# Performance work log

Measured on AMD Instinct MI355X. Metric: run time of the kernel, lower is better.

The kernel has to match this reference:

```python
import jax, jax.numpy as jnp
import numpy as np

RADIUS = 3
T_STEPS = 2
NEG = -9.0e8
B, L, DEG = 256, 64, 6
FEAT, BOND, FP, OUT = 39, 10, 256, 1


def _leaky(x):
    return jax.nn.leaky_relu(x, 0.01)


def _gru(x, h, wih, whh, bih, bhh):
    # PyTorch GRUCell: gates ordered (r, z, n)
    gi = x @ wih.T + bih
    gh = h @ whh.T + bhh
    ir, iz, inn = jnp.split(gi, 3, axis=-1)
    hr, hz, hn = jnp.split(gh, 3, axis=-1)
    r = jax.nn.sigmoid(ir + hr)
    z = jax.nn.sigmoid(iz + hz)
    n = jnp.tanh(inn + r * hn)
    return (1.0 - z) * n + z * h


def _forward(atom_list, bond_list, atom_mask,
             atom_fc_w, atom_fc_b, neighbor_fc_w, neighbor_fc_b,
             align_w, align_b, attend_w, attend_b,
             gru_wih, gru_whh, gru_bih, gru_bhh,
             mol_align_w, mol_align_b, mol_attend_w, mol_attend_b,
             mol_gru_wih, mol_gru_whh, mol_gru_bih, mol_gru_bhh,
             out_w, out_b,
             atom_degree_list, bond_degree_list):
    b, l, _ = atom_list.shape
    mask = atom_mask[..., None]                                   # [B,L,1]
    atom_feature = _leaky(atom_list @ atom_fc_w.T + atom_fc_b)    # [B,L,FP]

    # per-molecule neighbor gather (padding index = L-1)
    bidx = jnp.arange(b)[:, None, None]
    atom_nb = atom_list[bidx, atom_degree_list]                    # [B,L,deg,FEAT]
    bond_nb = bond_list[bidx, bond_degree_list]                    # [B,L,deg,BOND]
    neighbor_feature = _leaky(
        jnp.concatenate([atom_nb, bond_nb], axis=-1) @ neighbor_fc_w.T + neighbor_fc_b
    )                                                              # [B,L,deg,FP]

    attend_mask = (atom_degree_list != l - 1).astype(atom_feature.dtype)[..., None]
    softmax_mask = jnp.where(atom_degree_list == l - 1, NEG, 0.0).astype(atom_feature.dtype)[..., None]

    for d in range(RADIUS):
        af_exp = jnp.broadcast_to(atom_feature[:, :, None, :], neighbor_feature.shape)
        feature_align = jnp.concatenate([af_exp, neighbor_feature], axis=-1)  # [B,L,deg,2FP]
        align_score = _leaky(feature_align @ align_w[d].T + align_b[d]) + softmax_mask
        attention_weight = jax.nn.softmax(align_score, axis=-2) * attend_mask
        attended = neighbor_feature @ attend_w[d].T + attend_b[d]
        context = jax.nn.elu(jnp.sum(attention_weight * attended, axis=-2))   # [B,L,FP]
        atom_feature = _gru(context.reshape(b * l, -1), atom_feature.reshape(b * l, -1),
                            gru_wih[d], gru_whh[d], gru_bih[d], gru_bhh[d]).reshape(b, l, -1)
        # faithful to original: self-feature broadcast across neighbor dim
        neighbor_feature = jnp.broadcast_to(jax.nn.relu(atom_feature)[:, :, None, :],
                                            neighbor_feature.shape)

    mol_feature = jnp.sum(jax.nn.relu(atom_feature) * mask, axis=-2)          # [B,FP]
    mol_softmax_mask = jnp.where(atom_mask == 0, NEG, 0.0).astype(atom_feature.dtype)[..., None]

    for _ in range(T_STEPS):
        m_exp = jnp.broadcast_to(mol_feature[:, None, :], atom_feature.shape)
        mol_align = jnp.concatenate([m_exp, atom_feature], axis=-1)           # [B,L,2FP]
        mol_score = _leaky(mol_align @ mol_align_w.T + mol_align_b) + mol_softmax_mask
        mol_w = jax.nn.softmax(mol_score, axis=-2) * mask
        attended = atom_feature @ mol_attend_w.T + mol_attend_b
        mol_context = jax.nn.elu(jnp.sum(mol_w * attended, axis=-2))
        mol_feature = _gru(mol_context, mol_feature,
                           mol_gru_wih, mol_gru_whh, mol_gru_bih, mol_gru_bhh)

    mol_prediction = mol_feature @ out_w.T + out_b
    return atom_feature, mol_prediction


def setup_inputs() -> dict:
    key = jax.random.key(0)
    ks = jax.random.split(key, 20)
    s = 0.05
    return {
        "atom_list": jax.random.normal(ks[0], (B, L, FEAT), jnp.float32),
        "bond_list": jax.random.normal(ks[1], (B, L, BOND), jnp.float32),
        "atom_degree_list": jax.random.randint(ks[2], (B, L, DEG), 0, L),
        "bond_degree_list": jax.random.randint(ks[3], (B, L, DEG), 0, L),
        "atom_mask": jnp.ones((B, L), jnp.float32),
        "atom_fc_w": jax.random.normal(ks[4], (FP, FEAT)) * s,
        "atom_fc_b": jnp.zeros((FP,)),
        "neighbor_fc_w": jax.random.normal(ks[5], (FP, FEAT + BOND)) * s,
        "neighbor_fc_b": jnp.zeros((FP,)),
        "align_w": jax.random.normal(ks[6], (RADIUS, 1, 2 * FP)) * s,
        "align_b": jnp.zeros((RADIUS, 1)),
        "attend_w": jax.random.normal(ks[7], (RADIUS, FP, FP)) * s,
        "attend_b": jnp.zeros((RADIUS, FP)),
        "gru_wih": jax.random.normal(ks[8], (RADIUS, 3 * FP, FP)) * s,
        "gru_whh": jax.random.normal(ks[9], (RADIUS, 3 * FP, FP)) * s,
        "gru_bih": jnp.zeros((RADIUS, 3 * FP)),
        "gru_bhh": jnp.zeros((RADIUS, 3 * FP)),
        "mol_align_w": jax.random.normal(ks[10], (1, 2 * FP)) * s,
        "mol_align_b": jnp.zeros((1,)),
        "mol_attend_w": jax.random.normal(ks[11], (FP, FP)) * s,
        "mol_attend_b": jnp.zeros((FP,)),
        "mol_gru_wih": jax.random.normal(ks[12], (3 * FP, FP)) * s,
        "mol_gru_whh": jax.random.normal(ks[13], (3 * FP, FP)) * s,
        "mol_gru_bih": jnp.zeros((3 * FP,)),
        "mol_gru_bhh": jnp.zeros((3 * FP,)),
        "out_w": jax.random.normal(ks[14], (OUT, FP)) * s,
        "out_b": jnp.zeros((OUT,)),
    }


def reference(atom_list, bond_list, atom_degree_list, bond_degree_list, atom_mask,
              atom_fc_w, atom_fc_b, neighbor_fc_w, neighbor_fc_b,
              align_w, align_b, attend_w, attend_b,
              gru_wih, gru_whh, gru_bih, gru_bhh,
              mol_align_w, mol_align_b, mol_attend_w, mol_attend_b,
              mol_gru_wih, mol_gru_whh, mol_gru_bih, mol_gru_bhh,
              out_w, out_b):
    return _forward(atom_list, bond_list, atom_mask,
                    atom_fc_w, atom_fc_b, neighbor_fc_w, neighbor_fc_b,
                    align_w, align_b, attend_w, attend_b,
                    gru_wih, gru_whh, gru_bih, gru_bhh,
                    mol_align_w, mol_align_b, mol_attend_w, mol_attend_b,
                    mol_gru_wih, mol_gru_whh, mol_gru_bih, mol_gru_bhh,
                    out_w, out_b,
                    atom_degree_list, bond_degree_list)
```

## Files before the change

kernel.cpp:

```cpp
#include <hip/hip_runtime.h>
#include <hip/hip_bf16.h>

#define NB 256
#define NL 64
#define DEG 6
#define FEAT 39
#define BOND 10
#define FP 256
#define NEGV (-9.0e8f)

using s16x8 = __attribute__((ext_vector_type(8))) short;
using f32x4 = __attribute__((ext_vector_type(4))) float;

__device__ __forceinline__ unsigned short f2bf(float f){
  unsigned u = __float_as_uint(f);
  u += 0x7fffu + ((u >> 16) & 1u);
  return (unsigned short)(u >> 16);
}
__device__ __forceinline__ float lo16(unsigned u){ return __uint_as_float(u << 16); }
__device__ __forceinline__ float hi16(unsigned u){ return __uint_as_float(u & 0xffff0000u); }

__device__ __forceinline__ float block_sum256(float v, float* scr){
  #pragma unroll
  for(int o=32;o>0;o>>=1) v += __shfl_down(v, o, 64);
  __syncthreads();
  if((threadIdx.x & 63) == 0) scr[threadIdx.x >> 6] = v;
  __syncthreads();
  return scr[0] + scr[1] + scr[2] + scr[3];
}
__device__ __forceinline__ float wave_allsum(float v){
  #pragma unroll
  for(int o=1;o<64;o<<=1) v += __shfl_xor(v, o, 64);
  return v;
}

#define MCVT_N0 65536
#define MCVT_N1 196608
#define MCVT_N2 196608
#define MCVT_TOT (MCVT_N0+MCVT_N1+MCVT_N2)
#define CTXPK_N (3*8*8192)
#define GPK_N   (3*2*8*24576)
#define HALF_U16 24576

__global__ void k_cvt_mol(const float* __restrict__ a0, const float* __restrict__ a1,
                          const float* __restrict__ a2, unsigned short* __restrict__ dst){
  int i = blockIdx.x*256 + threadIdx.x;
  if(i >= MCVT_TOT) return;
  int off = i; const float* src;
  if(off < MCVT_N0) src = a0;
  else { off -= MCVT_N0;
    if(off < MCVT_N1) src = a1;
    else { off -= MCVT_N1; src = a2; } }
  dst[i] = f2bf(src[off]);
}

__global__ void k_pack(const float* __restrict__ attend_w, const float* __restrict__ gru_wih,
                       const float* __restrict__ gru_whh,
                       unsigned short* __restrict__ ctx_pk, unsigned short* __restrict__ gates_pk){
  int i = blockIdx.x*256 + threadIdx.x;
  if(i < CTXPK_N){
    int d = i >> 16;
    int rem = i & 65535;
    int kk = rem >> 13;
    int r2 = rem & 8191;
    int g = r2 >> 9;
    int l = (r2 >> 3) & 63;
    int q = r2 & 7;
    int row = g*16 + (l & 15);
    int k = kk*32 + (l >> 4)*8 + q;
    ctx_pk[i] = f2bf(attend_w[((size_t)d*256 + row)*256 + k]);
  } else {
    int j = i - CTXPK_N;
    if(j >= GPK_N) return;
    int d = j / 393216;
    int rem = j - d*393216;
    int nc = rem / 196608; rem -= nc*196608;
    int kk = rem / 24576;  rem -= kk*24576;
    int f = rem >> 9;
    int l = (rem >> 3) & 63;
    int q = rem & 7;
    int s = f >> 3, g = f & 7;
    int row = nc*128 + g*16 + (l & 15);
    int k = kk*32 + (l >> 4)*8 + q;
    float v = (s < 3) ? gru_wih[(((size_t)d*3 + s)*256 + row)*256 + k]
                      : gru_whh[(((size_t)d*3 + (s-3))*256 + row)*256 + k];
    gates_pk[j] = f2bf(v);
  }
}

__global__ void k_tr(const float* __restrict__ aw, const float* __restrict__ nw,
                     float* __restrict__ afcT, unsigned short* __restrict__ nfcT){
  int i = blockIdx.x*256 + threadIdx.x;
  if(i < 40*256){
    int k = i >> 8, r = i & 255;
    afcT[i] = (k < FEAT) ? aw[r*FEAT + k] : 0.f;
  } else {
    int j = i - 40*256;
    int k = j >> 8, r = j & 255;
    nfcT[j] = (k < FEAT+BOND) ? f2bf(nw[r*(FEAT+BOND) + k]) : (unsigned short)0;
  }
}

__global__ __launch_bounds__(256) void k_atom4(const float* __restrict__ atom,
    const float* __restrict__ afcT, const float* __restrict__ bias, float* __restrict__ af){
  __shared__ float WT[40*256];
  __shared__ float x_s[4][40];
  const int t = threadIdx.x, bl0 = blockIdx.x*4;
  for(int v=t; v<2560; v+=256) *(float4*)&WT[v*4] = *(const float4*)&afcT[v*4];
  for(int idx=t; idx<4*FEAT; idx+=256){ int a=idx/FEAT, k=idx%FEAT; x_s[a][k]=atom[(bl0+a)*FEAT+k]; }
  if(t < 4) x_s[t][39] = 0.f;
  __syncthreads();
  const int w = t>>6, t0 = (t&63)*4, row = bl0 + w;
  float4 b4 = *(const float4*)&bias[t0];
  float acc[4] = {b4.x, b4.y, b4.z, b4.w};
  for(int k=0;k<40;++k){
    float iv = x_s[w][k];
    float4 wv = *(const float4*)&WT[(k<<8)+t0];
    acc[0]=fmaf(iv,wv.x,acc[0]); acc[1]=fmaf(iv,wv.y,acc[1]);
    acc[2]=fmaf(iv,wv.z,acc[2]); acc[3]=fmaf(iv,wv.w,acc[3]);
  }
  float4 o;
  o.x = acc[0]>0.f?acc[0]:0.01f*acc[0]; o.y = acc[1]>0.f?acc[1]:0.01f*acc[1];
  o.z = acc[2]>0.f?acc[2]:0.01f*acc[2]; o.w = acc[3]>0.f?acc[3]:0.01f*acc[3];
  *(float4*)&af[(size_t)row*FP + t0] = o;
}

__global__ __launch_bounds__(256) void k_nbr4(const float* __restrict__ atom,
    const float* __restrict__ bond, const int* __restrict__ adl, const int* __restrict__ bdl,
    const unsigned short* __restrict__ nfcT, const float* __restrict__ bn,
    const float* __restrict__ alw, const float* __restrict__ alb,
    const float* __restrict__ af, float* __restrict__ wnf, float* __restrict__ swb){
  __shared__ unsigned short WnT[52*256];
  __shared__ float in_s[4][DEG][52];
  __shared__ int   ai_s[4][DEG];
  const int t = threadIdx.x, bl0 = blockIdx.x*4;
  if(t < 24){ int a=t/6, d=t%6; ai_s[a][d] = adl[(bl0+a)*DEG + d]; }
  for(int v=t; v<1664; v+=256) *(s16x8*)&WnT[v*8] = *(const s16x8*)&nfcT[v*8];
  __syncthreads();
  for(int idx=t; idx<4*DEG*(FEAT+BOND); idx+=256){
    int a = idx/(DEG*(FEAT+BOND)), rem = idx%(DEG*(FEAT+BOND));
    int d = rem/(FEAT+BOND), k = rem%(FEAT+BOND);
    int bb = (bl0+a) >> 6;
    float v;
    if(k < FEAT) v = atom[((size_t)bb*NL + ai_s[a][d])*FEAT + k];
    else { int bi = bdl[(bl0+a)*DEG + d]; v = bond[((size_t)bb*NL + bi)*BOND + (k-FEAT)]; }
    in_s[a][d][k] = v;
  }
  if(t < 24){ int a=t/6, d=t%6; in_s[a][d][49]=0.f; in_s[a][d][50]=0.f; in_s[a][d][51]=0.f; }
  __syncthreads();
  const int w = t>>6, lane = t&63, t0 = lane*4, row = bl0 + w;
  float acc[DEG][4] = {};
  for(int k=0;k<52;++k){
    uint2 u = *(const uint2*)&WnT[(k<<8) + t0];
    float w0=lo16(u.x), w1=hi16(u.x), w2=lo16(u.y), w3=hi16(u.y);
    #pragma unroll
    for(int d=0;d<DEG;++d){
      float iv = in_s[w][d][k];
      acc[d][0]=fmaf(iv,w0,acc[d][0]); acc[d][1]=fmaf(iv,w1,acc[d][1]);
      acc[d][2]=fmaf(iv,w2,acc[d][2]); acc[d][3]=fmaf(iv,w3,acc[d][3]);
    }
  }
  float4 bnv = *(const float4*)&bn[t0];
  float bna[4] = {bnv.x, bnv.y, bnv.z, bnv.w};
  float nf[DEG][4];
  #pragma unroll
  for(int d=0;d<DEG;++d)
    #pragma unroll
    for(int j=0;j<4;++j){ float v = acc[d][j] + bna[j]; nf[d][j] = v>0.f ? v : 0.01f*v; }
  float4 af4 = *(const float4*)&af[(size_t)row*FP + t0];
  float4 a1  = *(const float4*)&alw[t0];
  float4 a2  = *(const float4*)&alw[FP + t0];
  float sa = wave_allsum(af4.x*a1.x + af4.y*a1.y + af4.z*a1.z + af4.w*a1.w);
  float sd[DEG];
  #pragma unroll
  for(int d=0;d<DEG;++d)
    sd[d] = wave_allsum(nf[d][0]*a2.x + nf[d][1]*a2.y + nf[d][2]*a2.z + nf[d][3]*a2.w);
  float ab = alb[0];
  float sc[DEG], msk[DEG];
  #pragma unroll
  for(int d=0;d<DEG;++d){
    float v = sa + sd[d] + ab;
    v = v>0.f ? v : 0.01f*v;
    msk[d] = (ai_s[w][d] == NL-1) ? 0.f : 1.f;
    sc[d] = v + (msk[d] > 0.f ? 0.f : NEGV);
  }
  float m = sc[0];
  #pragma unroll
  for(int d=1;d<DEG;++d) m = fmaxf(m, sc[d]);
  float e[DEG], Z = 0.f;
  #pragma unroll
  for(int d=0;d<DEG;++d){ e[d] = expf(sc[d]-m); Z += e[d]; }
  float wgt[DEG], sw = 0.f;
  #pragma unroll
  for(int d=0;d<DEG;++d){ wgt[d] = e[d]/Z*msk[d]; sw += wgt[d]; }
  float o[4] = {};
  #pragma unroll
  for(int d=0;d<DEG;++d)
    #pragma unroll
    for(int j=0;j<4;++j) o[j] = fmaf(wgt[d], nf[d][j], o[j]);
  float4 ov; ov.x=o[0]; ov.y=o[1]; ov.z=o[2]; ov.w=o[3];
  *(float4*)&wnf[(size_t)row*FP + t0] = ov;
  if(lane == 0) swb[row] = sw;
}

__global__ __launch_bounds__(512) void k_radius2(
    const float* __restrict__ wnf, float* __restrict__ af, const float* __restrict__ swb,
    const unsigned short* __restrict__ ctx_pk, const unsigned short* __restrict__ gates_pk,
    const float* __restrict__ attend_b,
    const float* __restrict__ gru_bih, const float* __restrict__ gru_bhh){
  __shared__ __align__(16) unsigned short Cf[32*512];
  __shared__ __align__(16) unsigned short Bu[2][HALF_U16];
  const int t = threadIdx.x;
  const int w = t>>6, lane = t&63, lr = lane&15, ks = lane>>4;
  const int wm = w>>2, wn = w&3;
  const int m0 = blockIdx.x*64;

  s16x8 pf[6]; int pfn = 2;
  auto LOADT = [&](const unsigned short* src, int n){
    pfn = n;
    #pragma unroll
    for(int c=0;c<6;++c) if(c < n) pf[c] = *(const s16x8*)(src + (w + c*8)*512 + lane*8);
  };
  auto WRITET = [&](int h){
    #pragma unroll
    for(int c=0;c<6;++c) if(c < pfn) *(s16x8*)&Bu[h][(w + c*8)*512 + lane*8] = pf[c];
  };

  LOADT(ctx_pk, 2);
  WRITET(0);
  int half = 0;

  for(int d=0; d<3; ++d){
    const float* bat  = attend_b + d*256;
    const float* bihd = gru_bih + d*768;
    const float* bhhd = gru_bhh + d*768;
    f32x4 acc2[2][4] = {};
    for(int kk=0; kk<8; ++kk){
      __syncthreads();
      if(kk < 7) LOADT(ctx_pk + ((size_t)d*8 + kk+1)*8192, 2);
      else       LOADT(gates_pk + ((size_t)(d*2 + 0)*8 + 0)*24576, 6);
      s16x8 xf[2];
      #pragma unroll
      for(int mf=0; mf<2; ++mf){
        int row = m0 + wm*32 + mf*16 + lr;
        float4 v0, v1;
        if(d == 0){
          const float* sp = wnf + (size_t)row*256 + kk*32 + ks*8;
          v0 = *(const float4*)sp; v1 = *(const float4*)(sp+4);
        } else {
          const float* sp = af + (size_t)row*256 + kk*32 + ks*8;
          v0 = *(const float4*)sp; v1 = *(const float4*)(sp+4);
          float sw = swb[row];
          v0.x=fmaxf(v0.x,0.f)*sw; v0.y=fmaxf(v0.y,0.f)*sw;
          v0.z=fmaxf(v0.z,0.f)*sw; v0.w=fmaxf(v0.w,0.f)*sw;
          v1.x=fmaxf(v1.x,0.f)*sw; v1.y=fmaxf(v1.y,0.f)*sw;
          v1.z=fmaxf(v1.z,0.f)*sw; v1.w=fmaxf(v1.w,0.f)*sw;
        }
        unsigned short tmp[8] = {f2bf(v0.x),f2bf(v0.y),f2bf(v0.z),f2bf(v0.w),
                                 f2bf(v1.x),f2bf(v1.y),f2bf(v1.z),f2bf(v1.w)};
        xf[mf] = *(s16x8*)tmp;
      }
      #pragma unroll
      for(int nf=0; nf<4; ++nf){
        s16x8 wf = *(const s16x8*)&Bu[half][((wn*4 + nf)*64 + lane)*8];
        acc2[0][nf] = __builtin_amdgcn_mfma_f32_16x16x32_bf16(wf, xf[0], acc2[0][nf],0,0,0);
        acc2[1][nf] = __builtin_amdgcn_mfma_f32_16x16x32_bf16(wf, xf[1], acc2[1][nf],0,0,0);
      }
      WRITET(half^1);
      half ^= 1;
    }
    #pragma unroll
    for(int mf=0; mf<2; ++mf){
      float swv = swb[m0 + wm*32 + mf*16 + lr];
      #pragma unroll
      for(int nf=0; nf<4; ++nf){
        int nb = wn*64 + nf*16 + ks*4;
        float4 b4 = *(const float4*)&bat[nb];
        float bj[4] = {b4.x, b4.y, b4.z, b4.w};
        unsigned short o4[4];
        #pragma unroll
        for(int j=0;j<4;++j){
          float v = acc2[mf][nf][j] + swv*bj[j];
          v = v > 0.f ? v : expm1f(v);
          o4[j] = f2bf(v);
        }
        int gm = wm*2 + mf;
        int kkp = wn*2 + (nf>>1);
        int lhi = ((nf & 1) << 1) | (ks >> 1);
        int addr = (gm*8 + kkp)*512 + (lhi*16 + lr)*8 + (ks & 1)*4;
        *(uint2*)&Cf[addr] = *(uint2*)o4;
      }
    }
    float hnew0[2][2][4];
    for(int nc=0; nc<2; ++nc){
      f32x4 aR[2][2] = {}, aZ[2][2] = {}, aN[2][2] = {}, aH[2][2] = {};
      for(int kk=0; kk<8; ++kk){
        __syncthreads();
        bool last = (nc == 1) && (kk == 7);
        if(!last){
          if(kk < 7)      LOADT(gates_pk + ((size_t)(d*2 + nc)*8 + kk+1)*24576, 6);
          else            LOADT(gates_pk + ((size_t)(d*2 + 1)*8 + 0)*24576, 6);
        } else if(d < 2){
          LOADT(ctx_pk + ((size_t)(d+1)*8 + 0)*8192, 2);
        }
        s16x8 hf[2];
        #pragma unroll
        for(int mf=0; mf<2; ++mf){
          int row = m0 + wm*32 + mf*16 + lr;
          const float* sp = af + (size_t)row*256 + kk*32 + ks*8;
          float4 v0 = *(const float4*)sp, v1 = *(const float4*)(sp+4);
          unsigned short tmp[8] = {f2bf(v0.x),f2bf(v0.y),f2bf(v0.z),f2bf(v0.w),
                                   f2bf(v1.x),f2bf(v1.y),f2bf(v1.z),f2bf(v1.w)};
          hf[mf] = *(s16x8*)tmp;
        }
        s16x8 cf0 = *(const s16x8*)&Cf[((wm*2 + 0)*8 + kk)*512 + lane*8];
        s16x8 cf1 = *(const s16x8*)&Cf[((wm*2 + 1)*8 + kk)*512 + lane*8];
        #pragma unroll
        for(int fn=0; fn<2; ++fn){
          int g = wn*2 + fn;
          s16x8 b0 = *(const s16x8*)&Bu[half][((0*8 + g)*64 + lane)*8];
          s16x8 b1 = *(const s16x8*)&Bu[half][((1*8 + g)*64 + lane)*8];
          s16x8 b2 = *(const s16x8*)&Bu[half][((2*8 + g)*64 + lane)*8];
          s16x8 b3 = *(const s16x8*)&Bu[half][((3*8 + g)*64 + lane)*8];
          s16x8 b4 = *(const s16x8*)&Bu[half][((4*8 + g)*64 + lane)*8];
          s16x8 b5 = *(const s16x8*)&Bu[half][((5*8 + g)*64 + lane)*8];
          aR[0][fn] = __builtin_amdgcn_mfma_f32_16x16x32_bf16(cf0, b0, aR[0][fn],0,0,0);
          aR[1][fn] = __builtin_amdgcn_mfma_f32_16x16x32_bf16(cf1, b0, aR[1][fn],0,0,0);
          aZ[0][fn] = __builtin_amdgcn_mfma_f32_16x16x32_bf16(cf0, b1, aZ[0][fn],0,0,0);
          aZ[1][fn] = __builtin_amdgcn_mfma_f32_16x16x32_bf16(cf1, b1, aZ[1][fn],0,0,0);
          aN[0][fn] = __builtin_amdgcn_mfma_f32_16x16x32_bf16(cf0, b2, aN[0][fn],0,0,0);
          aN[1][fn] = __builtin_amdgcn_mfma_f32_16x16x32_bf16(cf1, b2, aN[1][fn],0,0,0);
          aR[0][fn] = __builtin_amdgcn_mfma_f32_16x16x32_bf16(hf[0], b3, aR[0][fn],0,0,0);
          aR[1][fn] = __builtin_amdgcn_mfma_f32_16x16x32_bf16(hf[1], b3, aR[1][fn],0,0,0);
          aZ[0][fn] = __builtin_amdgcn_mfma_f32_16x16x32_bf16(hf[0], b4, aZ[0][fn],0,0,0);
          aZ[1][fn] = __builtin_amdgcn_mfma_f32_16x16x32_bf16(hf[1], b4, aZ[1][fn],0,0,0);
          aH[0][fn] = __builtin_amdgcn_mfma_f32_16x16x32_bf16(hf[0], b5, aH[0][fn],0,0,0);
          aH[1][fn] = __builtin_amdgcn_mfma_f32_16x16x32_bf16(hf[1], b5, aH[1][fn],0,0,0);
        }
        if(!last || d < 2) WRITET(half^1);
        half ^= 1;
      }
      if(nc == 0){
        #pragma unroll
        for(int mf=0; mf<2; ++mf)
          #pragma unroll
          for(int fn=0; fn<2; ++fn){
            int n = wn*32 + fn*16 + lr;
            float brz = bihd[n] + bhhd[n];
            float bzz = bihd[256+n] + bhhd[256+n];
            float bnn = bihd[512+n];
            float bhn = bhhd[512+n];
            #pragma unroll
            for(int j=0;j<4;++j){
              int m = m0 + wm*32 + mf*16 + ks*4 + j;
              float hold = af[(size_t)m*256 + n];
              float r = 1.f/(1.f + expf(-(aR[mf][fn][j] + brz)));
              float z = 1.f/(1.f + expf(-(aZ[mf][fn][j] + bzz)));
              float ng = tanhf(aN[mf][fn][j] + bnn + r*(aH[mf][fn][j] + bhn));
              hnew0[mf][fn][j] = (1.f - z)*ng + z*hold;
            }
          }
      } else {
        #pragma unroll
        for(int mf=0; mf<2; ++mf)
          #pragma unroll
          for(int fn=0; fn<2; ++fn){
            int n = 128 + wn*32 + fn*16 + lr;
            float brz = bihd[n] + bhhd[n];
            float bzz = bihd[256+n] + bhhd[256+n];
            float bnn = bihd[512+n];
            float bhn = bhhd[512+n];
            #pragma unroll
            for(int j=0;j<4;++j){
              int m = m0 + wm*32 + mf*16 + ks*4 + j;
              float hold = af[(size_t)m*256 + n];
              float r = 1.f/(1.f + expf(-(aR[mf][fn][j] + brz)));
              float z = 1.f/(1.f + expf(-(aZ[mf][fn][j] + bzz)));
              float ng = tanhf(aN[mf][fn][j] + bnn + r*(aH[mf][fn][j] + bhn));
              af[(size_t)m*256 + n] = (1.f - z)*ng + z*hold;
            }
          }
        #pragma unroll
        for(int mf=0; mf<2; ++mf)
          #pragma unroll
          for(int fn=0; fn<2; ++fn){
            int n = wn*32 + fn*16 + lr;
            #pragma unroll
            for(int j=0;j<4;++j){
              int m = m0 + wm*32 + mf*16 + ks*4 + j;
              af[(size_t)m*256 + n] = hnew0[mf][fn][j];
            }
          }
      }
    }
  }
}

__global__ __launch_bounds__(256) void k_lin_gemm(
    const float* __restrict__ Xsrc, const unsigned short* __restrict__ Wbf,
    const float* __restrict__ bias, float* __restrict__ Y){
  __shared__ unsigned short A_lds[64][264];
  __shared__ unsigned short B_lds[64][264];
  const int t = threadIdx.x;
  const int m0 = (blockIdx.x >> 2) * 64, n0 = (blockIdx.x & 3) * 64;
  const int rb = t >> 4, cb = (t & 15) * 16;
  for(int i=0;i<4;++i){
    int row = i*16 + rb;
    const float* src = Xsrc + (size_t)(m0+row)*FP + cb;
    unsigned short tmp[16];
    #pragma unroll
    for(int q=0;q<4;++q){
      float4 v = ((const float4*)src)[q];
      tmp[q*4+0]=f2bf(v.x); tmp[q*4+1]=f2bf(v.y); tmp[q*4+2]=f2bf(v.z); tmp[q*4+3]=f2bf(v.w);
    }
    *(s16x8*)&A_lds[row][cb]   = *(s16x8*)&tmp[0];
    *(s16x8*)&A_lds[row][cb+8] = *(s16x8*)&tmp[8];
    const unsigned short* wsrc = Wbf + (size_t)(n0+row)*FP + cb;
    *(s16x8*)&B_lds[row][cb]   = *(const s16x8*)&wsrc[0];
    *(s16x8*)&B_lds[row][cb+8] = *(const s16x8*)&wsrc[8];
  }
  __syncthreads();
  const int w = t>>6, lane = t&63, lr = lane&15, ks = lane>>4;
  const int wr = (w>>1)*32, wc = (w&1)*32;
  f32x4 acc[2][2] = {};
  #pragma unroll
  for(int kk=0;kk<8;++kk){
    int ko = kk*32 + ks*8;
    s16x8 a0 = *(const s16x8*)&A_lds[wr+lr][ko];
    s16x8 a1 = *(const s16x8*)&A_lds[wr+16+lr][ko];
    s16x8 b0 = *(const s16x8*)&B_lds[wc+lr][ko];
    s16x8 b1 = *(const s16x8*)&B_lds[wc+16+lr][ko];
    acc[0][0] = __builtin_amdgcn_mfma_f32_16x16x32_bf16(a0,b0,acc[0][0],0,0,0);
    acc[0][1] = __builtin_amdgcn_mfma_f32_16x16x32_bf16(a0,b1,acc[0][1],0,0,0);
    acc[1][0] = __builtin_amdgcn_mfma_f32_16x16x32_bf16(a1,b0,acc[1][0],0,0,0);
    acc[1][1] = __builtin_amdgcn_mfma_f32_16x16x32_bf16(a1,b1,acc[1][1],0,0,0);
  }
  #pragma unroll
  for(int fm=0;fm<2;++fm)
    #pragma unroll
    for(int fn=0;fn<2;++fn){
      int n = n0 + wc + fn*16 + lr;
      float bv = bias[n];
      #pragma unroll
      for(int j=0;j<4;++j){
        int m = m0 + wr + fm*16 + ks*4 + j;
        Y[(size_t)m*FP + n] = acc[fm][fn][j] + bv;
      }
    }
}

__global__ __launch_bounds__(256) void k_gates32(
    const unsigned short* __restrict__ ctxbf, const float* __restrict__ h_glob,
    const unsigned short* __restrict__ wihbf, const unsigned short* __restrict__ whhbf,
    const float* __restrict__ bih, const float* __restrict__ bhh,
    float* __restrict__ h_out){
  __shared__ unsigned short A_ctx[32][40];
  __shared__ unsigned short A_h[32][40];
  __shared__ unsigned short B_lds[6][64][40];
  const int t = threadIdx.x;
  const int m0 = (blockIdx.x >> 2) * 32, nc = (blockIdx.x & 3) * 64;
  const int w = t>>6, lane = t&63, lr = lane&15, ks = lane>>4;
  const int mh = (w>>1)*16, nh = (w&1)*32;
  f32x4 acc[6][2] = {};
  for(int kk=0;kk<8;++kk){
    const int k0 = kk*32;
    __syncthreads();
    {
      int row = t>>3, c4 = (t&7)*4;
      *(uint2*)&A_ctx[row][c4] = *(const uint2*)(ctxbf + (size_t)(m0+row)*FP + k0 + c4);
      float4 hv = *(const float4*)(h_glob + (size_t)(m0+row)*FP + k0 + c4);
      unsigned short ht[4] = {f2bf(hv.x), f2bf(hv.y), f2bf(hv.z), f2bf(hv.w)};
      *(uint2*)&A_h[row][c4] = *(uint2*)ht;
    }
    #pragma unroll
    for(int i=0;i<6;++i){
      int idx = i*256 + t;
      int s = idx >> 8, rem = idx & 255;
      int row = rem >> 2, c8 = (rem & 3)*8;
      const unsigned short* wsrc = (s < 3)
          ? wihbf + (size_t)(s*FP + nc + row)*FP + k0 + c8
          : whhbf + (size_t)((s-3)*FP + nc + row)*FP + k0 + c8;
      *(s16x8*)&B_lds[s][row][c8] = *(const s16x8*)wsrc;
    }
    __syncthreads();
    s16x8 ac = *(const s16x8*)&A_ctx[mh+lr][ks*8];
    s16x8 ah = *(const s16x8*)&A_h[mh+lr][ks*8];
    #pragma unroll
    for(int s=0;s<6;++s){
      s16x8 a = (s < 3) ? ac : ah;
      #pragma unroll
      for(int fn=0;fn<2;++fn){
        s16x8 b = *(const s16x8*)&B_lds[s][nh+fn*16+lr][ks*8];
        acc[s][fn] = __builtin_amdgcn_mfma_f32_16x16x32_bf16(a,b,acc[s][fn],0,0,0);
      }
    }
  }
  #pragma unroll
  for(int fn=0;fn<2;++fn){
    int n = nc + nh + fn*16 + lr;
    float bir = bih[n], biz = bih[FP+n], bin_ = bih[2*FP+n];
    float bhr = bhh[n], bhz = bhh[FP+n], bhn  = bhh[2*FP+n];
    #pragma unroll
    for(int j=0;j<4;++j){
      int m = m0 + mh + ks*4 + j;
      float h = h_glob[(size_t)m*FP + n];
      float ir = acc[0][fn][j]+bir, iz = acc[1][fn][j]+biz, inn = acc[2][fn][j]+bin_;
      float hr = acc[3][fn][j]+bhr, hz = acc[4][fn][j]+bhz, hn  = acc[5][fn][j]+bhn;
      float r = 1.f/(1.f + expf(-(ir+hr)));
      float z = 1.f/(1.f + expf(-(iz+hz)));
      float ng = tanhf(inn + r*hn);
      h_out[(size_t)m*FP + n] = (1.f-z)*ng + z*h;
    }
  }
}

__global__ void k_finalize(const float* __restrict__ af, const float* __restrict__ mask,
                           float* __restrict__ molfeat, float* __restrict__ out_af){
  const int b = blockIdx.x, t = threadIdx.x;
  __shared__ float msk_s[NL];
  if(t < NL) msk_s[t] = mask[b*NL + t];
  __syncthreads();
  float mf = 0.f;
  for(int l=0;l<NL;++l){
    float v = af[(size_t)(b*NL + l)*FP + t];
    out_af[(size_t)(b*NL + l)*FP + t] = v;
    mf = fmaf(fmaxf(v,0.f), msk_s[l], mf);
  }
  molfeat[b*FP + t] = mf;
}

__global__ void k_mol_ctx(const float* __restrict__ af, const float* __restrict__ att,
    const float* __restrict__ mfin, const float* __restrict__ maw,
    const float* __restrict__ mabp, const float* __restrict__ mask,
    unsigned short* __restrict__ ctxb){
  const int b = blockIdx.x, t = threadIdx.x;
  __shared__ float mf_s[FP];
  __shared__ float sc_s[NL], aw_s[NL], scr[4];
  mf_s[t] = mfin[b*FP + t];
  __syncthreads();
  float sa = block_sum256(maw[t]*mf_s[t], scr);
  int l = t >> 2, q = t & 3;
  float p = 0.f;
  {
    const float4* ar = (const float4*)(af + (size_t)(b*NL + l)*FP + q*64);
    const float4* w2 = (const float4*)(maw + FP + q*64);
    #pragma unroll
    for(int k=0;k<16;++k){
// ... 218 lines not shown
    float rg = 1.f/(1.f + expf(-(ir+hr)));
    float zg = 1.f/(1.f + expf(-(iz+hz)));
    float ng = tanhf(inn + rg*hn);
    af[(size_t)(row0+r)*FP + t] = (1.f-zg)*ng + zg*h_s[r][t];
  }
}

__global__ void k_mol_att(const float* __restrict__ af, const float* __restrict__ maw,
    const float* __restrict__ mab, const float* __restrict__ mask,
    float* __restrict__ att, float* __restrict__ molfeat, float* __restrict__ out_af){
  const int b = blockIdx.x, t = threadIdx.x;
  __shared__ __align__(16) float a_s[32][FP];
  __shared__ float msk_s[NL];
  if(t < NL) msk_s[t] = mask[b*NL + t];
  __syncthreads();
  float mf = 0.f;
  const float4* wr = (const float4*)(maw + (size_t)t*FP);
  float mabv = mab[t];
  for(int half=0; half<2; ++half){
    #pragma unroll
    for(int i=0;i<32;++i){
      int l = half*32 + i;
      float v = af[(size_t)(b*NL + l)*FP + t];
      a_s[i][t] = v;
      out_af[(size_t)(b*NL + l)*FP + t] = v;
      mf = fmaf(fmaxf(v,0.f), msk_s[l], mf);
    }
    __syncthreads();
    float acc[32];
    #pragma unroll
    for(int i=0;i<32;++i) acc[i] = 0.f;
    for(int k4=0;k4<FP/4;++k4){
      float4 w = wr[k4];
      #pragma unroll
      for(int i=0;i<32;++i){
        float4 xv = ((const float4*)a_s[i])[k4];
        acc[i] = fmaf(xv.x,w.x,acc[i]); acc[i] = fmaf(xv.y,w.y,acc[i]);
        acc[i] = fmaf(xv.z,w.z,acc[i]); acc[i] = fmaf(xv.w,w.w,acc[i]);
      }
    }
    #pragma unroll
    for(int i=0;i<32;++i) att[(size_t)(b*NL + half*32 + i)*FP + t] = acc[i] + mabv;
    __syncthreads();
  }
  molfeat[b*FP + t] = mf;
}

__global__ void k_mol_step(const float* __restrict__ af, const float* __restrict__ att,
    float* __restrict__ molfeat, const float* __restrict__ maw, const float* __restrict__ mabp,
    const float* __restrict__ mask,
    const float* __restrict__ wih, const float* __restrict__ whh,
    const float* __restrict__ bih, const float* __restrict__ bhh){
  const int b = blockIdx.x, t = threadIdx.x;
  __shared__ __align__(16) float mf_s[FP];
  __shared__ __align__(16) float ctx_s[FP];
  __shared__ float sc_s[NL], aw_s[NL], scr[4];
  mf_s[t] = molfeat[b*FP + t];
  __syncthreads();
  float sa = block_sum256(maw[t]*mf_s[t], scr);
  int l = t >> 2, q = t & 3;
  float p = 0.f;
  {
    const float* ar = af + (size_t)(b*NL + l)*FP + q*64;
    const float* w2 = maw + FP + q*64;
    for(int k=0;k<64;++k) p = fmaf(ar[k], w2[k], p);
  }
  p += __shfl_xor(p, 1, 64);
  p += __shfl_xor(p, 2, 64);
  if(q == 0){
    float mv = mask[b*NL + l];
    float v = sa + p + mabp[0];
    v = v > 0.f ? v : 0.01f*v;
    sc_s[l] = v + (mv == 0.f ? NEGV : 0.f);
  }
  __syncthreads();
  if(t < NL){
    float s = sc_s[t];
    float m = s;
    #pragma unroll
    for(int o=32;o>0;o>>=1) m = fmaxf(m, __shfl_xor(m, o, 64));
    float e = expf(s - m);
    float Z = e;
    #pragma unroll
    for(int o=32;o>0;o>>=1) Z += __shfl_xor(Z, o, 64);
    aw_s[t] = e / Z * mask[b*NL + t];
  }
  __syncthreads();
  float acc = 0.f;
  for(int l2=0;l2<NL;++l2) acc = fmaf(aw_s[l2], att[(size_t)(b*NL + l2)*FP + t], acc);
  ctx_s[t] = acc > 0.f ? acc : expm1f(acc);
  __syncthreads();
  float air=0.f, aiz=0.f, ain=0.f, ahr=0.f, ahz=0.f, ahn=0.f;
  const float4* wirp=(const float4*)(wih + (size_t)t*FP);
  const float4* wizp=(const float4*)(wih + (size_t)(FP+t)*FP);
  const float4* winp=(const float4*)(wih + (size_t)(2*FP+t)*FP);
  const float4* whrp=(const float4*)(whh + (size_t)t*FP);
  const float4* whzp=(const float4*)(whh + (size_t)(FP+t)*FP);
  const float4* whnp=(const float4*)(whh + (size_t)(2*FP+t)*FP);
  for(int k4=0;k4<FP/4;++k4){
    float4 xv = ((const float4*)ctx_s)[k4];
    float4 hv = ((const float4*)mf_s)[k4];
    float4 f0=wirp[k4], f1=wizp[k4], f2=winp[k4];
    float4 g0=whrp[k4], g1=whzp[k4], g2=whnp[k4];
    air=fmaf(xv.x,f0.x,air); air=fmaf(xv.y,f0.y,air); air=fmaf(xv.z,f0.z,air); air=fmaf(xv.w,f0.w,air);
    aiz=fmaf(xv.x,f1.x,aiz); aiz=fmaf(xv.y,f1.y,aiz); aiz=fmaf(xv.z,f1.z,aiz); aiz=fmaf(xv.w,f1.w,aiz);
    ain=fmaf(xv.x,f2.x,ain); ain=fmaf(xv.y,f2.y,ain); ain=fmaf(xv.z,f2.z,ain); ain=fmaf(xv.w,f2.w,ain);
    ahr=fmaf(hv.x,g0.x,ahr); ahr=fmaf(hv.y,g0.y,ahr); ahr=fmaf(hv.z,g0.z,ahr); ahr=fmaf(hv.w,g0.w,ahr);
    ahz=fmaf(hv.x,g1.x,ahz); ahz=fmaf(hv.y,g1.y,ahz); ahz=fmaf(hv.z,g1.z,ahz); ahz=fmaf(hv.w,g1.w,ahz);
    ahn=fmaf(hv.x,g2.x,ahn); ahn=fmaf(hv.y,g2.y,ahn); ahn=fmaf(hv.z,g2.z,ahn); ahn=fmaf(hv.w,g2.w,ahn);
  }
  float ir=air+bih[t], iz=aiz+bih[FP+t], inn=ain+bih[2*FP+t];
  float hr=ahr+bhh[t], hz=ahz+bhh[FP+t], hn=ahn+bhh[2*FP+t];
  float rg = 1.f/(1.f + expf(-(ir+hr)));
  float zg = 1.f/(1.f + expf(-(iz+hz)));
  float ng = tanhf(inn + rg*hn);
  molfeat[b*FP + t] = (1.f-zg)*ng + zg*mf_s[t];
}

extern "C" void kernel_launch(void* const* d_in, const int* in_sizes, int n_in,
                              void* d_out, int out_size, void* d_ws, size_t ws_size,
                              hipStream_t stream){
  const float* atom_list = (const float*)d_in[0];
  const float* bond_list = (const float*)d_in[1];
  const int*   adl       = (const int*)d_in[2];
  const int*   bdl       = (const int*)d_in[3];
  const float* amask     = (const float*)d_in[4];
  const float* afc_w     = (const float*)d_in[5];
  const float* afc_b     = (const float*)d_in[6];
  const float* nfc_w     = (const float*)d_in[7];
  const float* nfc_b     = (const float*)d_in[8];
  const float* align_w   = (const float*)d_in[9];
  const float* align_b   = (const float*)d_in[10];
  const float* attend_w  = (const float*)d_in[11];
  const float* attend_b  = (const float*)d_in[12];
  const float* gru_wih   = (const float*)d_in[13];
  const float* gru_whh   = (const float*)d_in[14];
  const float* gru_bih   = (const float*)d_in[15];
  const float* gru_bhh   = (const float*)d_in[16];
  const float* mol_align_w  = (const float*)d_in[17];
  const float* mol_align_b  = (const float*)d_in[18];
  const float* mol_attend_w = (const float*)d_in[19];
  const float* mol_attend_b = (const float*)d_in[20];
  const float* mg_wih    = (const float*)d_in[21];
  const float* mg_whh    = (const float*)d_in[22];
  const float* mg_bih    = (const float*)d_in[23];
  const float* mg_bhh    = (const float*)d_in[24];
  const float* out_w     = (const float*)d_in[25];
  const float* out_b     = (const float*)d_in[26];

  float* out_af   = (float*)d_out;
  float* out_pred = out_af + (size_t)NB*NL*FP;

  const size_t NROW = (size_t)NB*NL;
  const size_t F32_CNT = 2*NROW*FP + NROW + 2*(size_t)NB*FP + 40*256;
  const size_t U16_CNT = (size_t)NB*FP + MCVT_TOT + 52*256 + CTXPK_N + GPK_N;
  const size_t NEED = F32_CNT*4 + U16_CNT*2;

  if(ws_size >= NEED){
    float* af_a    = (float*)d_ws;
    float* wnf     = af_a + NROW*FP;
    float* swb     = wnf  + NROW*FP;
    float* mf_a    = swb  + NROW;
    float* mf_b    = mf_a + (size_t)NB*FP;
    float* afcT    = mf_b + (size_t)NB*FP;
    unsigned short* ctxbf_m = (unsigned short*)(afcT + 40*256);
    unsigned short* maw_bf  = ctxbf_m + (size_t)NB*FP;
    unsigned short* mgih_bf = maw_bf + MCVT_N0;
    unsigned short* mghh_bf = mgih_bf + MCVT_N1;
    unsigned short* nfcT_bf = mghh_bf + MCVT_N2;
    unsigned short* ctx_pk  = nfcT_bf + 52*256;
    unsigned short* gates_pk= ctx_pk + CTXPK_N;

    k_cvt_mol<<<(MCVT_TOT+255)/256, 256, 0, stream>>>(mol_attend_w, mg_wih, mg_whh, maw_bf);
    k_pack<<<(CTXPK_N+GPK_N)/256, 256, 0, stream>>>(attend_w, gru_wih, gru_whh, ctx_pk, gates_pk);
    k_tr<<<(40*256 + 52*256)/256, 256, 0, stream>>>(afc_w, nfc_w, afcT, nfcT_bf);

    k_atom4<<<NB*NL/4, 256, 0, stream>>>(atom_list, afcT, afc_b, af_a);
    k_nbr4<<<NB*NL/4, 256, 0, stream>>>(atom_list, bond_list, adl, bdl,
                                        nfcT_bf, nfc_b, align_w, align_b, af_a, wnf, swb);
    k_radius2<<<NB*NL/64, 512, 0, stream>>>(wnf, af_a, swb, ctx_pk, gates_pk,
                                            attend_b, gru_bih, gru_bhh);
    k_lin_gemm<<<(NB*NL/64)*4, 256, 0, stream>>>(af_a, maw_bf, mol_attend_b, wnf);
    k_finalize<<<NB, 256, 0, stream>>>(af_a, amask, mf_a, out_af);
    float* m_cur = mf_a; float* m_nxt = mf_b;
    for(int s=0; s<2; ++s){
      k_mol_ctx<<<NB, 256, 0, stream>>>(af_a, wnf, m_cur, mol_align_w, mol_align_b,
                                        amask, ctxbf_m);
      k_gates32<<<(NB/32)*4, 256, 0, stream>>>(ctxbf_m, m_cur, mgih_bf, mghh_bf,
                                               mg_bih, mg_bhh, m_nxt);
      float* tmp = m_cur; m_cur = m_nxt; m_nxt = tmp;
    }
    k_out<<<NB, 256, 0, stream>>>(m_cur, out_w, out_b, out_pred);
  } else {
    float* af      = (float*)d_ws;
    float* wnf     = af  + NROW*FP;
    float* swb     = wnf + NROW*FP;
    float* molfeat = swb + NROW;

    k_atom_fc<<<NB*NL, FP, 0, stream>>>(atom_list, afc_w, afc_b, af);
    k_nbr_align<<<NB*NL, FP, 0, stream>>>(atom_list, bond_list, adl, bdl,
                                          nfc_w, nfc_b, align_w, align_b, af, wnf, swb);
    for(int d=0; d<3; ++d){
      const float* Wat = attend_w + (size_t)d*FP*FP;
      const float* bat = attend_b + (size_t)d*FP;
      const float* wih = gru_wih + (size_t)d*3*FP*FP;
      const float* whh = gru_whh + (size_t)d*3*FP*FP;
      const float* bih = gru_bih + (size_t)d*3*FP;
      const float* bhh = gru_bhh + (size_t)d*3*FP;
      if(d == 0) k_ctx_gru<0><<<NB*NL/16, FP, 0, stream>>>(wnf, swb, af, Wat, bat, wih, whh, bih, bhh);
      else       k_ctx_gru<1><<<NB*NL/16, FP, 0, stream>>>(af,  swb, af, Wat, bat, wih, whh, bih, bhh);
    }
    k_mol_att<<<NB, FP, 0, stream>>>(af, mol_attend_w, mol_attend_b, amask, wnf, molfeat, out_af);
    for(int s=0; s<2; ++s)
      k_mol_step<<<NB, FP, 0, stream>>>(af, wnf, molfeat, mol_align_w, mol_align_b, amask,
                                        mg_wih, mg_whh, mg_bih, mg_bhh);
    k_out<<<NB, FP, 0, stream>>>(molfeat, out_w, out_b, out_pred);
  }
}
```

Baseline: 323.6 us.

## Split GRU gate tiles into four column chunks with ping-pong hidden buffers

The fused radius kernel now processes the GRU gate GEMM in four 64-column chunks instead of two 128-column chunks. This halves the shared-memory weight tile, prefetch registers and accumulators so that more blocks can be resident (launch bounds now request 4 blocks). Hidden states ping-pong between two global buffers, so each chunk can write new h directly without holding the first half in registers. The cost is more chunk iterations, more barriers and re-reading the hidden-state and context fragments per chunk, plus an extra workspace buffer.

```diff
diff --git a/kernel.cpp b/kernel.cpp
--- a/kernel.cpp
+++ b/kernel.cpp
@@ -38,9 +38,10 @@
 #define MCVT_N1 196608
 #define MCVT_N2 196608
 #define MCVT_TOT (MCVT_N0+MCVT_N1+MCVT_N2)
-#define CTXPK_N (3*8*8192)
-#define GPK_N   (3*2*8*24576)
-#define HALF_U16 24576
+#define CT_U16 8192
+#define GT_U16 12288
+#define CTXPK_N (3*8*CT_U16)
+#define GPK_N   (3*4*8*GT_U16)
 
 __global__ void k_cvt_mol(const float* __restrict__ a0, const float* __restrict__ a1,
                           const float* __restrict__ a2, unsigned short* __restrict__ dst){
@@ -74,13 +75,13 @@
     if(j >= GPK_N) return;
     int d = j / 393216;
     int rem = j - d*393216;
-    int nc = rem / 196608; rem -= nc*196608;
-    int kk = rem / 24576;  rem -= kk*24576;
+    int nc = rem / 98304;  rem -= nc*98304;
+    int kk = rem / 12288;  rem -= kk*12288;
     int f = rem >> 9;
     int l = (rem >> 3) & 63;
     int q = rem & 7;
-    int s = f >> 3, g = f & 7;
-    int row = nc*128 + g*16 + (l & 15);
+    int s = f >> 2, gl = f & 3;
+    int row = nc*64 + gl*16 + (l & 15);
     int k = kk*32 + (l >> 4)*8 + q;
     float v = (s < 3) ? gru_wih[(((size_t)d*3 + s)*256 + row)*256 + k]
                       : gru_whh[(((size_t)d*3 + (s-3))*256 + row)*256 + k];
@@ -203,32 +204,39 @@
   if(lane == 0) swb[row] = sw;
 }
 
-__global__ __launch_bounds__(512) void k_radius2(
-    const float* __restrict__ wnf, float* __restrict__ af, const float* __restrict__ swb,
+__global__ __launch_bounds__(512, 4) void k_radius3(
+    const float* __restrict__ wnf, float* __restrict__ af_a, float* __restrict__ af_b,
+    const float* __restrict__ swb,
     const unsigned short* __restrict__ ctx_pk, const unsigned short* __restrict__ gates_pk,
     const float* __restrict__ attend_b,
     const float* __restrict__ gru_bih, const float* __restrict__ gru_bhh){
   __shared__ __align__(16) unsigned short Cf[32*512];
-  __shared__ __align__(16) unsigned short Bu[2][HALF_U16];
+  __shared__ __align__(16) unsigned short Bu[2][GT_U16];
   const int t = threadIdx.x;
   const int w = t>>6, lane = t&63, lr = lane&15, ks = lane>>4;
   const int wm = w>>2, wn = w&3;
   const int m0 = blockIdx.x*64;
 
-  s16x8 pf[6]; int pfn = 2;
+  s16x8 pf[3]; int pfn = 2;
   auto LOADT = [&](const unsigned short* src, int n){
     pfn = n;
     #pragma unroll
-    for(int c=0;c<6;++c) if(c < n) pf[c] = *(const s16x8*)(src + (w + c*8)*512 + lane*8);
+    for(int c=0;c<3;++c) if(c < n) pf[c] = *(const s16x8*)(src + (w + c*8)*512 + lane*8);
   };
   auto WRITET = [&](int h){
     #pragma unroll
-    for(int c=0;c<6;++c) if(c < pfn) *(s16x8*)&Bu[h][(w + c*8)*512 + lane*8] = pf[c];
+    for(int c=0;c<3;++c) if(c < pfn) *(s16x8*)&Bu[h][(w + c*8)*512 + lane*8] = pf[c];
   };
 
   LOADT(ctx_pk, 2);
   WRITET(0);
   int half = 0;
+  const float* hc = af_a;
+  float*       hn = af_b;
+
+  float swv[2];
+  swv[0] = swb[m0 + wm*32 + lr];
+  swv[1] = swb[m0 + wm*32 + 16 + lr];
 
   for(int d=0; d<3; ++d){
     const float* bat  = attend_b + d*256;
@@ -237,8 +245,8 @@
     f32x4 acc2[2][4] = {};
     for(int kk=0; kk<8; ++kk){
       __syncthreads();
-      if(kk < 7) LOADT(ctx_pk + ((size_t)d*8 + kk+1)*8192, 2);
-      else       LOADT(gates_pk + ((size_t)(d*2 + 0)*8 + 0)*24576, 6);
+      if(kk < 7) LOADT(ctx_pk + ((size_t)d*8 + kk+1)*CT_U16, 2);
+      else       LOADT(gates_pk + ((size_t)(d*4 + 0)*8 + 0)*GT_U16, 3);
       s16x8 xf[2];
       #pragma unroll
       for(int mf=0; mf<2; ++mf){
@@ -248,9 +256,9 @@
           const float* sp = wnf + (size_t)row*256 + kk*32 + ks*8;
           v0 = *(const float4*)sp; v1 = *(const float4*)(sp+4);
         } else {
-          const float* sp = af + (size_t)row*256 + kk*32 + ks*8;
+          const float* sp = hc + (size_t)row*256 + kk*32 + ks*8;
           v0 = *(const float4*)sp; v1 = *(const float4*)(sp+4);
-          float sw = swb[row];
+          float sw = swv[mf];
           v0.x=fmaxf(v0.x,0.f)*sw; v0.y=fmaxf(v0.y,0.f)*sw;
           v0.z=fmaxf(v0.z,0.f)*sw; v0.w=fmaxf(v0.w,0.f)*sw;
           v1.x=fmaxf(v1.x,0.f)*sw; v1.y=fmaxf(v1.y,0.f)*sw;
@@ -271,7 +279,7 @@
     }
     #pragma unroll
     for(int mf=0; mf<2; ++mf){
-      float swv = swb[m0 + wm*32 + mf*16 + lr];
+      float swvv = swv[mf];
       #pragma unroll
       for(int nf=0; nf<4; ++nf){
         int nb = wn*64 + nf*16 + ks*4;
@@ -280,7 +288,7 @@
         unsigned short o4[4];
         #pragma unroll
         for(int j=0;j<4;++j){
-          float v = acc2[mf][nf][j] + swv*bj[j];
+          float v = acc2[mf][nf][j] + swvv*bj[j];
           v = v > 0.f ? v : expm1f(v);
           o4[j] = f2bf(v);
         }
@@ -291,23 +299,22 @@
         *(uint2*)&Cf[addr] = *(uint2*)o4;
       }
     }
-    float hnew0[2][2][4];
-    for(int nc=0; nc<2; ++nc){
-      f32x4 aR[2][2] = {}, aZ[2][2] = {}, aN[2][2] = {}, aH[2][2] = {};
+    for(int nc=0; nc<4; ++nc){
+      f32x4 aR[2] = {}, aZ[2] = {}, aN[2] = {}, aH[2] = {};
       for(int kk=0; kk<8; ++kk){
         __syncthreads();
-        bool last = (nc == 1) && (kk == 7);
+        bool last = (nc == 3) && (kk == 7);
         if(!last){
-          if(kk < 7)      LOADT(gates_pk + ((size_t)(d*2 + nc)*8 + kk+1)*24576, 6);
-          else            LOADT(gates_pk + ((size_t)(d*2 + 1)*8 + 0)*24576, 6);
+          if(kk < 7) LOADT(gates_pk + ((size_t)(d*4 + nc)*8 + kk+1)*GT_U16, 3);
+          else       LOADT(gates_pk + ((size_t)(d*4 + nc+1)*8 + 0)*GT_U16, 3);
         } else if(d < 2){
-          LOADT(ctx_pk + ((size_t)(d+1)*8 + 0)*8192, 2);
+          LOADT(ctx_pk + ((size_t)(d+1)*8 + 0)*CT_U16, 2);
         }
         s16x8 hf[2];
         #pragma unroll
         for(int mf=0; mf<2; ++mf){
           int row = m0 + wm*32 + mf*16 + lr;
-          const float* sp = af + (size_t)row*256 + kk*32 + ks*8;
+          const float* sp = hc + (size_t)row*256 + kk*32 + ks*8;
           float4 v0 = *(const float4*)sp, v1 = *(const float4*)(sp+4);
           unsigned short tmp[8] = {f2bf(v0.x),f2bf(v0.y),f2bf(v0.z),f2bf(v0.w),
                                    f2bf(v1.x),f2bf(v1.y),f2bf(v1.z),f2bf(v1.w)};
@@ -315,84 +322,48 @@
         }
         s16x8 cf0 = *(const s16x8*)&Cf[((wm*2 + 0)*8 + kk)*512 + lane*8];
         s16x8 cf1 = *(const s16x8*)&Cf[((wm*2 + 1)*8 + kk)*512 + lane*8];
-        #pragma unroll
-        for(int fn=0; fn<2; ++fn){
-          int g = wn*2 + fn;
-          s16x8 b0 = *(const s16x8*)&Bu[half][((0*8 + g)*64 + lane)*8];
-          s16x8 b1 = *(const s16x8*)&Bu[half][((1*8 + g)*64 + lane)*8];
-          s16x8 b2 = *(const s16x8*)&Bu[half][((2*8 + g)*64 + lane)*8];
-          s16x8 b3 = *(const s16x8*)&Bu[half][((3*8 + g)*64 + lane)*8];
-          s16x8 b4 = *(const s16x8*)&Bu[half][((4*8 + g)*64 + lane)*8];
-          s16x8 b5 = *(const s16x8*)&Bu[half][((5*8 + g)*64 + lane)*8];
-          aR[0][fn] = __builtin_amdgcn_mfma_f32_16x16x32_bf16(cf0, b0, aR[0][fn],0,0,0);
-          aR[1][fn] = __builtin_amdgcn_mfma_f32_16x16x32_bf16(cf1, b0, aR[1][fn],0,0,0);
-          aZ[0][fn] = __builtin_amdgcn_mfma_f32_16x16x32_bf16(cf0, b1, aZ[0][fn],0,0,0);
-          aZ[1][fn] = __builtin_amdgcn_mfma_f32_16x16x32_bf16(cf1, b1, aZ[1][fn],0,0,0);
-          aN[0][fn] = __builtin_amdgcn_mfma_f32_16x16x32_bf16(cf0, b2, aN[0][fn],0,0,0);
-          aN[1][fn] = __builtin_amdgcn_mfma_f32_16x16x32_bf16(cf1, b2, aN[1][fn],0,0,0);
-          aR[0][fn] = __builtin_amdgcn_mfma_f32_16x16x32_bf16(hf[0], b3, aR[0][fn],0,0,0);
-          aR[1][fn] = __builtin_amdgcn_mfma_f32_16x16x32_bf16(hf[1], b3, aR[1][fn],0,0,0);
-          aZ[0][fn] = __builtin_amdgcn_mfma_f32_16x16x32_bf16(hf[0], b4, aZ[0][fn],0,0,0);
-          aZ[1][fn] = __builtin_amdgcn_mfma_f32_16x16x32_bf16(hf[1], b4, aZ[1][fn],0,0,0);
-          aH[0][fn] = __builtin_amdgcn_mfma_f32_16x16x32_bf16(hf[0], b5, aH[0][fn],0,0,0);
-          aH[1][fn] = __builtin_amdgcn_mfma_f32_16x16x32_bf16(hf[1], b5, aH[1][fn],0,0,0);
-        }
+        s16x8 b0 = *(const s16x8*)&Bu[half][((0*4 + wn)*64 + lane)*8];
+        s16x8 b1 = *(const s16x8*)&Bu[half][((1*4 + wn)*64 + lane)*8];
+        s16x8 b2 = *(const s16x8*)&Bu[half][((2*4 + wn)*64 + lane)*8];
+        s16x8 b3 = *(const s16x8*)&Bu[half][((3*4 + wn)*64 + lane)*8];
+        s16x8 b4 = *(const s16x8*)&Bu[half][((4*4 + wn)*64 + lane)*8];
+        s16x8 b5 = *(const s16x8*)&Bu[half][((5*4 + wn)*64 + lane)*8];
+        aR[0] = __builtin_amdgcn_mfma_f32_16x16x32_bf16(cf0, b0, aR[0],0,0,0);
+        aR[1] = __builtin_amdgcn_mfma_f32_16x16x32_bf16(cf1, b0, aR[1],0,0,0);
+        aZ[0] = __builtin_amdgcn_mfma_f32_16x16x32_bf16(cf0, b1, aZ[0],0,0,0);
+        aZ[1] = __builtin_amdgcn_mfma_f32_16x16x32_bf16(cf1, b1, aZ[1],0,0,0);
+        aN[0] = __builtin_amdgcn_mfma_f32_16x16x32_bf16(cf0, b2, aN[0],0,0,0);
+        aN[1] = __builtin_amdgcn_mfma_f32_16x16x32_bf16(cf1, b2, aN[1],0,0,0);
+        aR[0] = __builtin_amdgcn_mfma_f32_16x16x32_bf16(hf[0], b3, aR[0],0,0,0);
+        aR[1] = __builtin_amdgcn_mfma_f32_16x16x32_bf16(hf[1], b3, aR[1],0,0,0);
+        aZ[0] = __builtin_amdgcn_mfma_f32_16x16x32_bf16(hf[0], b4, aZ[0],0,0,0);
+        aZ[1] = __builtin_amdgcn_mfma_f32_16x16x32_bf16(hf[1], b4, aZ[1],0,0,0);
+        aH[0] = __builtin_amdgcn_mfma_f32_16x16x32_bf16(hf[0], b5, aH[0],0,0,0);
+        aH[1] = __builtin_amdgcn_mfma_f32_16x16x32_bf16(hf[1], b5, aH[1],0,0,0);
         if(!last || d < 2) WRITET(half^1);
         half ^= 1;
       }
-      if(nc == 0){
+      {
+        int n = nc*64 + wn*16 + lr;
+        float brz = bihd[n] + bhhd[n];
+        float bzz = bihd[256+n] + bhhd[256+n];
+        float bnn = bihd[512+n];
+        float bhn = bhhd[512+n];
         #pragma unroll
-        for(int mf=0; mf<2; ++mf)
+        for(int mf=0; mf<2; ++mf){
           #pragma unroll
-          for(int fn=0; fn<2; ++fn){
-            int n = wn*32 + fn*16 + lr;
-            float brz = bihd[n] + bhhd[n];
-            float bzz = bihd[256+n] + bhhd[256+n];
-            float bnn = bihd[512+n];
-            float bhn = bhhd[512+n];
-            #pragma unroll
-            for(int j=0;j<4;++j){
-              int m = m0 + wm*32 + mf*16 + ks*4 + j;
-              float hold = af[(size_t)m*256 + n];
-              float r = 1.f/(1.f + expf(-(aR[mf][fn][j] + brz)));
-              float z = 1.f/(1.f + expf(-(aZ[mf][fn][j] + bzz)));
-              float ng = tanhf(aN[mf][fn][j] + bnn + r*(aH[mf][fn][j] + bhn));
-              hnew0[mf][fn][j] = (1.f - z)*ng + z*hold;
-            }
+          for(int j=0;j<4;++j){
+            int m = m0 + wm*32 + mf*16 + ks*4 + j;
+            float hold = hc[(size_t)m*256 + n];
+            float r = 1.f/(1.f + expf(-(aR[mf][j] + brz)));
+            float z = 1.f/(1.f + expf(-(aZ[mf][j] + bzz)));
+            float ng = tanhf(aN[mf][j] + bnn + r*(aH[mf][j] + bhn));
+            hn[(size_t)m*256 + n] = (1.f - z)*ng + z*hold;
           }
-      } else {
-        #pragma unroll
-        for(int mf=0; mf<2; ++mf)
-          #pragma unroll
-          for(int fn=0; fn<2; ++fn){
-            int n = 128 + wn*32 + fn*16 + lr;
-            float brz = bihd[n] + bhhd[n];
-            float bzz = bihd[256+n] + bhhd[256+n];
-            float bnn = bihd[512+n];
-            float bhn = bhhd[512+n];
-            #pragma unroll
-            for(int j=0;j<4;++j){
-              int m = m0 + wm*32 + mf*16 + ks*4 + j;
-              float hold = af[(size_t)m*256 + n];
-              float r = 1.f/(1.f + expf(-(aR[mf][fn][j] + brz)));
-              float z = 1.f/(1.f + expf(-(aZ[mf][fn][j] + bzz)));
-              float ng = tanhf(aN[mf][fn][j] + bnn + r*(aH[mf][fn][j] + bhn));
-              af[(size_t)m*256 + n] = (1.f - z)*ng + z*hold;
-            }
-          }
-        #pragma unroll
-        for(int mf=0; mf<2; ++mf)
-          #pragma unroll
-          for(int fn=0; fn<2; ++fn){
-            int n = wn*32 + fn*16 + lr;
-            #pragma unroll
-            for(int j=0;j<4;++j){
-              int m = m0 + wm*32 + mf*16 + ks*4 + j;
-              af[(size_t)m*256 + n] = hnew0[mf][fn][j];
-            }
-          }
+        }
       }
     }
+    const float* tmp = hc; hc = hn; hn = (float*)tmp;
   }
 }
 
@@ -917,13 +888,14 @@
   float* out_pred = out_af + (size_t)NB*NL*FP;
 
   const size_t NROW = (size_t)NB*NL;
-  const size_t F32_CNT = 2*NROW*FP + NROW + 2*(size_t)NB*FP + 40*256;
+  const size_t F32_CNT = 3*NROW*FP + NROW + 2*(size_t)NB*FP + 40*256;
   const size_t U16_CNT = (size_t)NB*FP + MCVT_TOT + 52*256 + CTXPK_N + GPK_N;
   const size_t NEED = F32_CNT*4 + U16_CNT*2;
 
   if(ws_size >= NEED){
     float* af_a    = (float*)d_ws;
-    float* wnf     = af_a + NROW*FP;
+    float* af_b    = af_a + NROW*FP;
+    float* wnf     = af_b + NROW*FP;
     float* swb     = wnf  + NROW*FP;
     float* mf_a    = swb  + NROW;
     float* mf_b    = mf_a + (size_t)NB*FP;
@@ -943,13 +915,14 @@
     k_atom4<<<NB*NL/4, 256, 0, stream>>>(atom_list, afcT, afc_b, af_a);
     k_nbr4<<<NB*NL/4, 256, 0, stream>>>(atom_list, bond_list, adl, bdl,
                                         nfcT_bf, nfc_b, align_w, align_b, af_a, wnf, swb);
-    k_radius2<<<NB*NL/64, 512, 0, stream>>>(wnf, af_a, swb, ctx_pk, gates_pk,
+    k_radius3<<<NB*NL/64, 512, 0, stream>>>(wnf, af_a, af_b, swb, ctx_pk, gates_pk,
                                             attend_b, gru_bih, gru_bhh);
-    k_lin_gemm<<<(NB*NL/64)*4, 256, 0, stream>>>(af_a, maw_bf, mol_attend_b, wnf);
-    k_finalize<<<NB, 256, 0, stream>>>(af_a, amask, mf_a, out_af);
+    float* af_fin = af_b;
+    k_lin_gemm<<<(NB*NL/64)*4, 256, 0, stream>>>(af_fin, maw_bf, mol_attend_b, wnf);
+    k_finalize<<<NB, 256, 0, stream>>>(af_fin, amask, mf_a, out_af);
     float* m_cur = mf_a; float* m_nxt = mf_b;
     for(int s=0; s<2; ++s){
-      k_mol_ctx<<<NB, 256, 0, stream>>>(af_a, wnf, m_cur, mol_align_w, mol_align_b,
+      k_mol_ctx<<<NB, 256, 0, stream>>>(af_fin, wnf, m_cur, mol_align_w, mol_align_b,
                                         amask, ctxbf_m);
       k_gates32<<<(NB/32)*4, 256, 0, stream>>>(ctxbf_m, m_cur, mgih_bf, mghh_bf,
                                                mg_bih, mg_bhh, m_nxt);
```

After: 386.8 us. 19.5% more time.
